# Performance work log

Hardware: AMD Instinct MI355X
Metric: run time of the kernel (lower is better)

Reference implementation:

```python
import jax, jax.numpy as jnp
import numpy as np

N_NODES = 100000
N_EDGES = 1600000
IN_CH = 16
HID = 128
N_LAYERS = 4
OUT_CH = 3


def setup_inputs() -> dict:
    key = jax.random.key(0)
    ks = jax.random.split(key, 8)
    x = jax.random.normal(ks[0], (N_NODES, IN_CH), dtype=jnp.float32)
    edge_index = jax.random.randint(ks[1], (2, N_EDGES), 0, N_NODES, dtype=jnp.int64)
    # glorot-ish scaled params
    enc_W = jax.random.normal(ks[2], (IN_CH, HID), dtype=jnp.float32) * (1.0 / np.sqrt(IN_CH))
    enc_b = jnp.zeros((HID,), dtype=jnp.float32)
    conv_W = jax.random.normal(ks[3], (N_LAYERS, HID, HID), dtype=jnp.float32) * (1.0 / np.sqrt(HID))
    conv_b = jnp.zeros((N_LAYERS, HID), dtype=jnp.float32)
    dec_W = jax.random.normal(ks[4], (HID, OUT_CH), dtype=jnp.float32) * (1.0 / np.sqrt(HID))
    dec_b = jnp.zeros((OUT_CH,), dtype=jnp.float32)
    return {"x": x, "edge_index": edge_index, "enc_W": enc_W, "enc_b": enc_b,
            "conv_W": conv_W, "conv_b": conv_b, "dec_W": dec_W, "dec_b": dec_b}


def _gcn_forward(x, edge_index, enc_W, enc_b, conv_W, conv_b, dec_W, dec_b):
    n = x.shape[0]
    # PyG GCNConv: add self-loops, symmetric deg^-1/2 normalization
    loops = jnp.arange(n, dtype=edge_index.dtype)
    src = jnp.concatenate([edge_index[0], loops])  # [E+N]
    dst = jnp.concatenate([edge_index[1], loops])  # [E+N]
    deg = jax.ops.segment_sum(jnp.ones_like(dst, dtype=x.dtype), dst, num_segments=n)
    dinv = jnp.where(deg > 0, jax.lax.rsqrt(deg), 0.0)
    norm = (dinv[src] * dinv[dst])[:, None]  # [E+N, 1]

    h = jax.nn.relu(x @ enc_W + enc_b)  # encoder + ReLU
    for l in range(conv_W.shape[0]):
        hw = h @ conv_W[l]                      # [N, H] transform
        msg = hw[src] * norm                    # gather + normalize
        h = jax.ops.segment_sum(msg, dst, num_segments=n) + conv_b[l]
        h = jax.nn.relu(h)
    return h @ dec_W + dec_b  # decoder [N, 3]


def reference(x, edge_index, enc_W, enc_b, conv_W, conv_b, dec_W, dec_b):
    return _gcn_forward(x, edge_index, enc_W, enc_b, conv_W, conv_b, dec_W, dec_b)
```

## Files before the change

kernel.cpp:

```cpp
#include <hip/hip_runtime.h>


typedef float f32x4 __attribute__((ext_vector_type(4)));
typedef short bf16x8 __attribute__((ext_vector_type(8)));
typedef _Float16 h8 __attribute__((ext_vector_type(8)));
typedef unsigned short u16x8 __attribute__((ext_vector_type(8)));

#define BKT_CAP 6144

__device__ inline void split_bf16(float x, ushort& hi, ushort& lo) {
  union { float f; unsigned u; } a, b, c;
  a.f = x;
  unsigned r = a.u + 0x7fffu + ((a.u >> 16) & 1u);
  hi = (ushort)(r >> 16);
  b.u = ((unsigned)hi) << 16;
  c.f = x - b.f;
  unsigned r2 = c.u + 0x7fffu + ((c.u >> 16) & 1u);
  lo = (ushort)(r2 >> 16);
}

__device__ inline float bf2f(ushort h) {
  union { unsigned u; float f; } t;
  t.u = ((unsigned)h) << 16;
  return t.f;
}


__global__ __launch_bounds__(256) void k_bin(const int* __restrict__ src, const int* __restrict__ dst,
                                             int* __restrict__ bcnt, int2* __restrict__ ebuf, int E, int NB) {
  __shared__ int hist[512];
  __shared__ int lofs[512];
  int tid = threadIdx.x;
  int base = blockIdx.x * 4096;
  for (int i = tid; i < NB; i += 256) hist[i] = 0;
  __syncthreads();
  int2 rec[16];
  int bk[16];
#pragma unroll
  for (int j = 0; j < 16; j++) {
    int e = base + j * 256 + tid;
    bk[j] = -1;
    if (e < E) {
      int d = dst[e];
      rec[j] = make_int2(d, src[e]);
      bk[j] = d >> 8;
      atomicAdd(&hist[bk[j]], 1);
    }
  }
  __syncthreads();
  for (int i = tid; i < NB; i += 256) {
    int c = hist[i];
    lofs[i] = c ? atomicAdd(&bcnt[i], c) : 0;
    hist[i] = 0;
  }
  __syncthreads();
#pragma unroll
  for (int j = 0; j < 16; j++) {
    if (bk[j] >= 0) {
      int p = lofs[bk[j]] + atomicAdd(&hist[bk[j]], 1);
      if (p < BKT_CAP) ebuf[(size_t)bk[j] * BKT_CAP + p] = rec[j];
    }
  }
}

__global__ __launch_bounds__(256) void k_bucket_hist(const int2* __restrict__ ebuf, const int* __restrict__ bcnt,
                                                     int* __restrict__ cnt, int N) {
  __shared__ int h[256];
  int b = blockIdx.x, tid = threadIdx.x;
  h[tid] = 0;
  __syncthreads();
  int n = min(bcnt[b], BKT_CAP);
  const int2* eb = ebuf + (size_t)b * BKT_CAP;
  for (int i = tid; i < n; i += 256) atomicAdd(&h[eb[i].x & 255], 1);
  __syncthreads();
  int d = (b << 8) + tid;
  if (d < N) cnt[d] = h[tid];
}

__global__ __launch_bounds__(256) void k_bucket_fill(const int2* __restrict__ ebuf, const int* __restrict__ bcnt,
                                                     const int* __restrict__ rp, int* __restrict__ col, int N) {
  __shared__ int h[256];
  int b = blockIdx.x, tid = threadIdx.x;
  h[tid] = 0;
  __syncthreads();
  int n = min(bcnt[b], BKT_CAP);
  const int2* eb = ebuf + (size_t)b * BKT_CAP;
  for (int i = tid; i < n; i += 256) {
    int2 r = eb[i];
    int pos = rp[r.x] + atomicAdd(&h[r.x & 255], 1);
    col[pos] = r.y;
  }
}


__global__ __launch_bounds__(256) void k_scan_local(const int* __restrict__ cnt, int* __restrict__ rp,
                                                    int* __restrict__ bsums, int N) {
  int base = blockIdx.x * 4096 + threadIdx.x * 16;
  int v[16];
#pragma unroll
  for (int j = 0; j < 16; j++) { int i = base + j; v[j] = (i < N) ? cnt[i] : 0; }
  int tsum = 0;
#pragma unroll
  for (int j = 0; j < 16; j++) tsum += v[j];
  int l = threadIdx.x & 63, w = threadIdx.x >> 6;
  int s = tsum;
#pragma unroll
  for (int off = 1; off < 64; off <<= 1) { int t = __shfl_up(s, off); if (l >= off) s += t; }
  __shared__ int wsum[4];
  if (l == 63) wsum[w] = s;
  __syncthreads();
  int woff = 0;
  for (int i = 0; i < w; i++) woff += wsum[i];
  int run = woff + s - tsum;
#pragma unroll
  for (int j = 0; j < 16; j++) { int i = base + j; if (i < N) rp[i] = run; run += v[j]; }
  if (threadIdx.x == 255) bsums[blockIdx.x] = woff + s;
}

__global__ void k_scan_sums(const int* __restrict__ bsums, int* __restrict__ bsex,
                            int* __restrict__ rp, int nsb, int N) {
  if (threadIdx.x == 0 && blockIdx.x == 0) {
    int run = 0;
    for (int i = 0; i < nsb; i++) { bsex[i] = run; run += bsums[i]; }
    rp[N] = run;
  }
}

__global__ __launch_bounds__(256) void k_scan_add(const int* __restrict__ cnt, int* __restrict__ rp,
                                                  const int* __restrict__ bsex, float* __restrict__ dinv, int N) {
  int i = blockIdx.x * blockDim.x + threadIdx.x;
  if (i >= N) return;
  rp[i] = rp[i] + bsex[i >> 12];
  dinv[i] = 1.0f / sqrtf((float)(cnt[i] + 1));
}

__global__ __launch_bounds__(128) void k_prep_w(const float* __restrict__ convW, ushort* __restrict__ Whi,
                                                ushort* __restrict__ Wlo) {
  int lk = blockIdx.x;
  int l = lk >> 7, k = lk & 127, c = threadIdx.x;
  float x = convW[((size_t)l * 128 + k) * 128 + c];
  ushort hi, lo;
  split_bf16(x, hi, lo);
  size_t o = ((size_t)l * 128 + c) * 128 + k;
  Whi[o] = hi;
  Wlo[o] = lo;
}


__global__ __launch_bounds__(256) void k_encoder(const float* __restrict__ x, const float* __restrict__ W,
                                                 const float* __restrict__ b, ushort* __restrict__ Hhi,
                                                 ushort* __restrict__ Hlo, int N) {
  int node = blockIdx.x * 2 + (threadIdx.x >> 7);
  int c = threadIdx.x & 127;
  if (node >= N) return;
  const float* xr = x + (size_t)node * 16;
  float acc = b[c];
#pragma unroll
  for (int k = 0; k < 16; k++) acc = fmaf(xr[k], W[k * 128 + c], acc);
  acc = fmaxf(acc, 0.0f);
  ushort hi, lo;
  split_bf16(acc, hi, lo);
  Hhi[(size_t)node * 128 + c] = hi;
  Hlo[(size_t)node * 128 + c] = lo;
}

__global__ __launch_bounds__(512) void k_gemm_mfma(const ushort* __restrict__ Ahi, const ushort* __restrict__ Alo,
                                                   const ushort* __restrict__ Whi, const ushort* __restrict__ Wlo,
                                                   const float* __restrict__ dinv, _Float16* __restrict__ B, int N) {
  __shared__ __align__(16) ushort lds[4 * 128 * 64];
  const int tid = threadIdx.x;
  const int row0 = blockIdx.x * 128;
  const int w = tid >> 6, l = tid & 63;
  const int wm = w >> 1, wn = w & 1;
  const int lr = l & 15, lg = l >> 4;

  f32x4 zero4 = {0.0f, 0.0f, 0.0f, 0.0f};
  f32x4 acc[2][4];
#pragma unroll
  for (int m = 0; m < 2; m++)
#pragma unroll
    for (int n = 0; n < 4; n++) acc[m][n] = zero4;

  for (int half = 0; half < 2; half++) {
    uint4 v[8];
#pragma unroll
    for (int i = 0; i < 8; i++) {
      int g = tid + i * 512;
      int region = g >> 10;
      int idx = g & 1023;
      int row = idx >> 3;
      int c16 = idx & 7;
      const ushort* srcb;
      int grow = row;
      bool valid = true;
      if (region == 0) { srcb = Ahi; grow = row0 + row; valid = grow < N; }
      else if (region == 1) { srcb = Alo; grow = row0 + row; valid = grow < N; }
      else if (region == 2) { srcb = Whi; }
      else { srcb = Wlo; }
      v[i] = valid ? *reinterpret_cast<const uint4*>(srcb + (size_t)grow * 128 + half * 64 + c16 * 8)
                   : uint4{0u, 0u, 0u, 0u};
    }
    if (half) __syncthreads();
#pragma unroll
    for (int i = 0; i < 8; i++) {
      int g = tid + i * 512;
      int region = g >> 10;
      int idx = g & 1023;
      int row = idx >> 3;
      int c16 = idx & 7;
      int byte_off = region * 16384 + ((row * 128 + c16 * 16) ^ ((row & 7) << 4));
      *reinterpret_cast<uint4*>(reinterpret_cast<char*>(lds) + byte_off) = v[i];
    }
    __syncthreads();

#pragma unroll
    for (int ksl = 0; ksl < 2; ksl++) {
      int kb = (ksl * 32 + lg * 8) * 2;
      bf16x8 ah[2], al[2];
#pragma unroll
      for (int m = 0; m < 2; m++) {
        int row = wm * 32 + m * 16 + lr;
        int off = (row * 128 + kb) ^ ((row & 7) << 4);
        ah[m] = *reinterpret_cast<const bf16x8*>(reinterpret_cast<char*>(lds) + off);
        al[m] = *reinterpret_cast<const bf16x8*>(reinterpret_cast<char*>(lds) + 16384 + off);
      }
      bf16x8 wh[4], wl[4];
#pragma unroll
      for (int n = 0; n < 4; n++) {
        int colr = wn * 64 + n * 16 + lr;
        int off = (colr * 128 + kb) ^ ((colr & 7) << 4);
        wh[n] = *reinterpret_cast<const bf16x8*>(reinterpret_cast<char*>(lds) + 32768 + off);
        wl[n] = *reinterpret_cast<const bf16x8*>(reinterpret_cast<char*>(lds) + 49152 + off);
      }
#pragma unroll
      for (int m = 0; m < 2; m++)
#pragma unroll
        for (int n = 0; n < 4; n++) {
          acc[m][n] = __builtin_amdgcn_mfma_f32_16x16x32_bf16(al[m], wh[n], acc[m][n], 0, 0, 0);
          acc[m][n] = __builtin_amdgcn_mfma_f32_16x16x32_bf16(ah[m], wl[n], acc[m][n], 0, 0, 0);
          acc[m][n] = __builtin_amdgcn_mfma_f32_16x16x32_bf16(ah[m], wh[n], acc[m][n], 0, 0, 0);
        }
    }
  }

#pragma unroll
  for (int m = 0; m < 2; m++) {
    int rbase = row0 + wm * 32 + m * 16 + lg * 4;
#pragma unroll
    for (int r = 0; r < 4; r++) {
      int grow = rbase + r;
      if (grow < N) {
        float s = dinv[grow];
#pragma unroll
        for (int n = 0; n < 4; n++) {
          int colc = wn * 64 + n * 16 + lr;
          B[(size_t)grow * 128 + colc] = (_Float16)(acc[m][n][r] * s);
        }
      }
    }
  }
}

__global__ __launch_bounds__(256) void k_aggregate(const _Float16* __restrict__ B, const int* __restrict__ rp,
                                                   const int* __restrict__ col, const float* __restrict__ dinv,
                                                   const float* __restrict__ bias, ushort* __restrict__ Hhi,
                                                   ushort* __restrict__ Hlo, int N) {
  int w = threadIdx.x >> 6, l = threadIdx.x & 63;
  int d = blockIdx.x * 4 + w;
  if (d >= N) return;
  int g = l >> 4, c16 = l & 15;
  int choff = c16 * 8;

  float acc[8];
#pragma unroll
  for (int j = 0; j < 8; j++) acc[j] = 0.0f;

  if (g == 0) {
    h8 sv = *reinterpret_cast<const h8*>(B + (size_t)d * 128 + choff);
#pragma unroll
    for (int j = 0; j < 8; j++) acc[j] += (float)sv[j];
  }

  int e0 = rp[d], e1 = rp[d + 1];
  int e = e0 + g;
  for (; e + 4 < e1; e += 8) {
    int s0 = col[e], s1 = col[e + 4];
    h8 v0 = *reinterpret_cast<const h8*>(B + (size_t)s0 * 128 + choff);
    h8 v1 = *reinterpret_cast<const h8*>(B + (size_t)s1 * 128 + choff);
#pragma unroll
    for (int j = 0; j < 8; j++) acc[j] += (float)v0[j] + (float)v1[j];
  }
  if (e < e1) {
    int s0 = col[e];
    h8 v0 = *reinterpret_cast<const h8*>(B + (size_t)s0 * 128 + choff);
#pragma unroll
    for (int j = 0; j < 8; j++) acc[j] += (float)v0[j];
  }

#pragma unroll
  for (int j = 0; j < 8; j++) acc[j] += __shfl_xor(acc[j], 32);
#pragma unroll
  for (int j = 0; j < 8; j++) acc[j] += __shfl_xor(acc[j], 16);

  float dv = dinv[d];
  u16x8 hv, lv;
#pragma unroll
  for (int j = 0; j < 8; j++) {
    float o = fmaxf(fmaf(dv, acc[j], bias[choff + j]), 0.0f);
    ushort hi, lo;
    split_bf16(o, hi, lo);
    hv[j] = hi;
    lv[j] = lo;
  }
  if (g == 0) *reinterpret_cast<u16x8*>(&Hhi[(size_t)d * 128 + choff]) = hv;
  if (g == 1) *reinterpret_cast<u16x8*>(&Hlo[(size_t)d * 128 + choff]) = lv;
}

__global__ __launch_bounds__(256) void k_decoder(const ushort* __restrict__ Hhi, const ushort* __restrict__ Hlo,
                                                 const float* __restrict__ W, const float* __restrict__ b,
                                                 float* __restrict__ out, int N) {
  int w = threadIdx.x >> 6, l = threadIdx.x & 63;
  int node = blockIdx.x * 4 + w;
  if (node >= N) return;
  size_t base = (size_t)node * 128;
  float h0 = bf2f(Hhi[base + l]) + bf2f(Hlo[base + l]);
  float h1 = bf2f(Hhi[base + 64 + l]) + bf2f(Hlo[base + 64 + l]);
  float s0 = h0 * W[l * 3 + 0] + h1 * W[(l + 64) * 3 + 0];
  float s1 = h0 * W[l * 3 + 1] + h1 * W[(l + 64) * 3 + 1];
  float s2 = h0 * W[l * 3 + 2] + h1 * W[(l + 64) * 3 + 2];
#pragma unroll
  for (int o = 32; o > 0; o >>= 1) {
    s0 += __shfl_down(s0, o);
    s1 += __shfl_down(s1, o);
    s2 += __shfl_down(s2, o);
  }
  if (l == 0) {
    out[(size_t)node * 3 + 0] = s0 + b[0];
    out[(size_t)node * 3 + 1] = s1 + b[1];
    out[(size_t)node * 3 + 2] = s2 + b[2];
  }
}

extern "C" void kernel_launch(void* const* d_in, const int* in_sizes, int n_in,
                              void* d_out, int out_size, void* d_ws, size_t ws_size,
                              hipStream_t stream) {
  const float* x     = (const float*)d_in[0];
  const int*   ei    = (const int*)d_in[1];
  const float* encW  = (const float*)d_in[2];
  const float* encb  = (const float*)d_in[3];
  const float* convW = (const float*)d_in[4];
  const float* convb = (const float*)d_in[5];
  const float* decW  = (const float*)d_in[6];
  const float* decb  = (const float*)d_in[7];
  const int N = in_sizes[0] / 16;
  const int E = in_sizes[1] / 2;
  const int L = in_sizes[4] / (128 * 128);
  const int* src = ei;
  const int* dst = ei + E;
  const int NB = (N + 255) >> 8;

  char* p = (char*)d_ws;
  auto alloc = [&](size_t bytes) -> void* {
    void* q = (void*)p;
    p += (bytes + 255) & ~(size_t)255;
    return q;
  };
  int nsb = (N + 4095) >> 12;
  int*       cnt    = (int*)alloc((size_t)N * 4);
  int*       rp     = (int*)alloc((size_t)(N + 1) * 4);
  int*       bsums  = (int*)alloc((size_t)nsb * 4);
  int*       bsex   = (int*)alloc((size_t)nsb * 4);
  int*       bcnt   = (int*)alloc((size_t)NB * 4);
  float*     dinv   = (float*)alloc((size_t)N * 4);
  int*       colA   = (int*)alloc((size_t)E * 4);
  ushort*    Hhi    = (ushort*)alloc((size_t)N * 128 * 2);
  ushort*    Hlo    = (ushort*)alloc((size_t)N * 128 * 2);
  size_t bh_bytes   = (size_t)N * 128 * 2;
  size_t ebuf_bytes = (size_t)NB * BKT_CAP * 8;
  void*  bh_union   = alloc(bh_bytes > ebuf_bytes ? bh_bytes : ebuf_bytes);
  _Float16* Bh      = (_Float16*)bh_union;
  int2*     ebuf    = (int2*)bh_union;
  ushort*    Whi    = (ushort*)alloc((size_t)L * 128 * 128 * 2);
  ushort*    Wlo    = (ushort*)alloc((size_t)L * 128 * 128 * 2);

  hipMemsetAsync(bcnt, 0, (size_t)NB * 4, stream);
  k_bin<<<(E + 4095) / 4096, 256, 0, stream>>>(src, dst, bcnt, ebuf, E, NB);
  k_bucket_hist<<<NB, 256, 0, stream>>>(ebuf, bcnt, cnt, N);
  k_scan_local<<<nsb, 256, 0, stream>>>(cnt, rp, bsums, N);
  k_scan_sums<<<1, 1, 0, stream>>>(bsums, bsex, rp, nsb, N);
  k_scan_add<<<(N + 255) / 256, 256, 0, stream>>>(cnt, rp, bsex, dinv, N);
  k_bucket_fill<<<NB, 256, 0, stream>>>(ebuf, bcnt, rp, colA, N);
  k_prep_w<<<L * 128, 128, 0, stream>>>(convW, Whi, Wlo);
  k_encoder<<<(N + 1) / 2, 256, 0, stream>>>(x, encW, encb, Hhi, Hlo, N);
  int gblocks = (N + 127) / 128;
  for (int l = 0; l < L; l++) {
    k_gemm_mfma<<<gblocks, 512, 0, stream>>>(Hhi, Hlo, Whi + (size_t)l * 128 * 128,
                                             Wlo + (size_t)l * 128 * 128, dinv, Bh, N);
    k_aggregate<<<(N + 3) / 4, 256, 0, stream>>>(Bh, rp, colA, dinv, convb + l * 128, Hhi, Hlo, N);
  }
  k_decoder<<<(N + 3) / 4, 256, 0, stream>>>(Hhi, Hlo, decW, decb, (float*)d_out, N);
}
```

Measured before the change: 553.9 us.

## Pack edge records into 32 bits and accumulate aggregation in fp16 with deeper unroll

Bucketed edge records are packed into one 32-bit word (low 8 bits of the destination plus a 24-bit source id), halving the edge buffer traffic in the binning, histogram and fill kernels. The aggregation kernel now sums neighbour rows in packed fp16 vector adds instead of converting each value to fp32, and unrolls to four gathers per iteration to raise memory-level parallelism. The cost is lower accumulation precision for high-degree nodes and a 24-bit limit on node ids.

```diff
diff --git a/kernel.cpp b/kernel.cpp
--- a/kernel.cpp
+++ b/kernel.cpp
@@ -27,14 +27,14 @@
 
 
 __global__ __launch_bounds__(256) void k_bin(const int* __restrict__ src, const int* __restrict__ dst,
-                                             int* __restrict__ bcnt, int2* __restrict__ ebuf, int E, int NB) {
+                                             int* __restrict__ bcnt, unsigned* __restrict__ ebuf, int E, int NB) {
   __shared__ int hist[512];
   __shared__ int lofs[512];
   int tid = threadIdx.x;
   int base = blockIdx.x * 4096;
   for (int i = tid; i < NB; i += 256) hist[i] = 0;
   __syncthreads();
-  int2 rec[16];
+  unsigned rec[16];
   int bk[16];
 #pragma unroll
   for (int j = 0; j < 16; j++) {
@@ -42,7 +42,7 @@
     bk[j] = -1;
     if (e < E) {
       int d = dst[e];
-      rec[j] = make_int2(d, src[e]);
+      rec[j] = ((unsigned)(d & 255) << 24) | (unsigned)src[e];
       bk[j] = d >> 8;
       atomicAdd(&hist[bk[j]], 1);
     }
@@ -63,32 +63,33 @@
   }
 }
 
-__global__ __launch_bounds__(256) void k_bucket_hist(const int2* __restrict__ ebuf, const int* __restrict__ bcnt,
+__global__ __launch_bounds__(256) void k_bucket_hist(const unsigned* __restrict__ ebuf, const int* __restrict__ bcnt,
                                                      int* __restrict__ cnt, int N) {
   __shared__ int h[256];
   int b = blockIdx.x, tid = threadIdx.x;
   h[tid] = 0;
   __syncthreads();
   int n = min(bcnt[b], BKT_CAP);
-  const int2* eb = ebuf + (size_t)b * BKT_CAP;
-  for (int i = tid; i < n; i += 256) atomicAdd(&h[eb[i].x & 255], 1);
+  const unsigned* eb = ebuf + (size_t)b * BKT_CAP;
+  for (int i = tid; i < n; i += 256) atomicAdd(&h[eb[i] >> 24], 1);
   __syncthreads();
   int d = (b << 8) + tid;
   if (d < N) cnt[d] = h[tid];
 }
 
-__global__ __launch_bounds__(256) void k_bucket_fill(const int2* __restrict__ ebuf, const int* __restrict__ bcnt,
+__global__ __launch_bounds__(256) void k_bucket_fill(const unsigned* __restrict__ ebuf, const int* __restrict__ bcnt,
                                                      const int* __restrict__ rp, int* __restrict__ col, int N) {
   __shared__ int h[256];
   int b = blockIdx.x, tid = threadIdx.x;
   h[tid] = 0;
   __syncthreads();
   int n = min(bcnt[b], BKT_CAP);
-  const int2* eb = ebuf + (size_t)b * BKT_CAP;
+  const unsigned* eb = ebuf + (size_t)b * BKT_CAP;
   for (int i = tid; i < n; i += 256) {
-    int2 r = eb[i];
-    int pos = rp[r.x] + atomicAdd(&h[r.x & 255], 1);
-    col[pos] = r.y;
+    unsigned r = eb[i];
+    int dlow = r >> 24;
+    int pos = rp[(b << 8) + dlow] + atomicAdd(&h[dlow], 1);
+    col[pos] = (int)(r & 0xFFFFFFu);
   }
 }
 
@@ -271,32 +272,32 @@
   int g = l >> 4, c16 = l & 15;
   int choff = c16 * 8;
 
-  float acc[8];
-#pragma unroll
-  for (int j = 0; j < 8; j++) acc[j] = 0.0f;
-
-  if (g == 0) {
-    h8 sv = *reinterpret_cast<const h8*>(B + (size_t)d * 128 + choff);
-#pragma unroll
-    for (int j = 0; j < 8; j++) acc[j] += (float)sv[j];
-  }
+  h8 pacc = {(_Float16)0, (_Float16)0, (_Float16)0, (_Float16)0,
+             (_Float16)0, (_Float16)0, (_Float16)0, (_Float16)0};
+
+  if (g == 0)
+    pacc += *reinterpret_cast<const h8*>(B + (size_t)d * 128 + choff);
 
   int e0 = rp[d], e1 = rp[d + 1];
   int e = e0 + g;
-  for (; e + 4 < e1; e += 8) {
-    int s0 = col[e], s1 = col[e + 4];
+  for (; e + 12 < e1; e += 16) {
+    int s0 = col[e], s1 = col[e + 4], s2 = col[e + 8], s3 = col[e + 12];
     h8 v0 = *reinterpret_cast<const h8*>(B + (size_t)s0 * 128 + choff);
     h8 v1 = *reinterpret_cast<const h8*>(B + (size_t)s1 * 128 + choff);
-#pragma unroll
-    for (int j = 0; j < 8; j++) acc[j] += (float)v0[j] + (float)v1[j];
-  }
-  if (e < e1) {
+    h8 v2 = *reinterpret_cast<const h8*>(B + (size_t)s2 * 128 + choff);
+    h8 v3 = *reinterpret_cast<const h8*>(B + (size_t)s3 * 128 + choff);
+    h8 t01 = v0 + v1;
+    h8 t23 = v2 + v3;
+    pacc += t01 + t23;
+  }
+  for (; e < e1; e += 4) {
     int s0 = col[e];
-    h8 v0 = *reinterpret_cast<const h8*>(B + (size_t)s0 * 128 + choff);
-#pragma unroll
-    for (int j = 0; j < 8; j++) acc[j] += (float)v0[j];
-  }
-
+    pacc += *reinterpret_cast<const h8*>(B + (size_t)s0 * 128 + choff);
+  }
+
+  float acc[8];
+#pragma unroll
+  for (int j = 0; j < 8; j++) acc[j] = (float)pacc[j];
 #pragma unroll
   for (int j = 0; j < 8; j++) acc[j] += __shfl_xor(acc[j], 32);
 #pragma unroll
@@ -376,10 +377,10 @@
   ushort*    Hhi    = (ushort*)alloc((size_t)N * 128 * 2);
   ushort*    Hlo    = (ushort*)alloc((size_t)N * 128 * 2);
   size_t bh_bytes   = (size_t)N * 128 * 2;
-  size_t ebuf_bytes = (size_t)NB * BKT_CAP * 8;
+  size_t ebuf_bytes = (size_t)NB * BKT_CAP * 4;
   void*  bh_union   = alloc(bh_bytes > ebuf_bytes ? bh_bytes : ebuf_bytes);
   _Float16* Bh      = (_Float16*)bh_union;
-  int2*     ebuf    = (int2*)bh_union;
+  unsigned* ebuf    = (unsigned*)bh_union;
   ushort*    Whi    = (ushort*)alloc((size_t)L * 128 * 128 * 2);
   ushort*    Wlo    = (ushort*)alloc((size_t)L * 128 * 128 * 2);
 
```

Measured after the change: 564.2 us. About the same (+1.9%).
